# Optimization experiments

Measured on AMD Instinct MI355X. Metric: run time of the kernel, lower is better.

The kernel has to match this reference:

```python
import jax, jax.numpy as jnp
import numpy as np

L, H, D, V, TMAX = 12, 12, 768, 50257, 1024
B, T = 2, 1024
HD = D // H
EPS = 1e-5


def new_gelu(x):
    return 0.5 * x * (1.0 + jnp.tanh(jnp.sqrt(2.0 / jnp.pi) * (x + 0.044715 * x ** 3)))


def layer_norm(x, w, b):
    mu = jnp.mean(x, axis=-1, keepdims=True)
    var = jnp.var(x, axis=-1, keepdims=True)
    return (x - mu) * jax.lax.rsqrt(var + EPS) * w + b


def setup_inputs() -> dict:
    key = jax.random.key(0)
    ks = jax.random.split(key, 12)
    s = 0.02
    return {
        "idx": jax.random.randint(ks[0], (B, T), 0, V),
        "wte": jax.random.normal(ks[1], (V, D), jnp.float32) * s,
        "wpe": jax.random.normal(ks[2], (TMAX, D), jnp.float32) * s,
        "ln1_w": jnp.ones((L, D), jnp.float32),
        "ln1_b": jnp.zeros((L, D), jnp.float32),
        "attn_w": jax.random.normal(ks[3], (L, D, 3 * D), jnp.float32) * s,
        "attn_b": jnp.zeros((L, 3 * D), jnp.float32),
        "proj_w": jax.random.normal(ks[4], (L, D, D), jnp.float32) * (s / jnp.sqrt(2.0 * L)),
        "proj_b": jnp.zeros((L, D), jnp.float32),
        "ln2_w": jnp.ones((L, D), jnp.float32),
        "ln2_b": jnp.zeros((L, D), jnp.float32),
        "fc_w": jax.random.normal(ks[5], (L, D, 4 * D), jnp.float32) * s,
        "fc_b": jnp.zeros((L, 4 * D), jnp.float32),
        "fc2_w": jax.random.normal(ks[6], (L, 4 * D, D), jnp.float32) * (s / jnp.sqrt(2.0 * L)),
        "fc2_b": jnp.zeros((L, D), jnp.float32),
        "lnf_w": jnp.ones((D,), jnp.float32),
        "lnf_b": jnp.zeros((D,), jnp.float32),
        "lm_head_w": jax.random.normal(ks[7], (D, V), jnp.float32) * s,
    }


def _gpt_forward(idx, wte, wpe, ln1_w, ln1_b, attn_w, attn_b, proj_w, proj_b,
                 ln2_w, ln2_b, fc_w, fc_b, fc2_w, fc2_b, lnf_w, lnf_b, lm_head_w):
    b, t = idx.shape
    x = wte[idx] + wpe[:t][None, :, :]  # [B,T,D]
    causal = jnp.tril(jnp.ones((t, t), bool))  # [T,T]
    scale = 1.0 / jnp.sqrt(jnp.asarray(HD, x.dtype))

    layer_params = {
        "ln1_w": ln1_w, "ln1_b": ln1_b, "attn_w": attn_w, "attn_b": attn_b,
        "proj_w": proj_w, "proj_b": proj_b, "ln2_w": ln2_w, "ln2_b": ln2_b,
        "fc_w": fc_w, "fc_b": fc_b, "fc2_w": fc2_w, "fc2_b": fc2_b,
    }

    def block(x, p):
        h = layer_norm(x, p["ln1_w"], p["ln1_b"])
        qkv = h @ p["attn_w"] + p["attn_b"]  # [B,T,3D]
        q, k, v = jnp.split(qkv, 3, axis=-1)
        q = q.reshape(b, t, H, HD)
        k = k.reshape(b, t, H, HD)
        v = v.reshape(b, t, H, HD)
        att = jnp.einsum("bqhd,bkhd->bhqk", q, k) * scale
        att = jnp.where(causal[None, None, :, :], att, -jnp.inf)
        att = jax.nn.softmax(att, axis=-1)
        y = jnp.einsum("bhqk,bkhd->bqhd", att, v).reshape(b, t, D)
        x = x + y @ p["proj_w"] + p["proj_b"]
        h2 = layer_norm(x, p["ln2_w"], p["ln2_b"])
        m = new_gelu(h2 @ p["fc_w"] + p["fc_b"])
        x = x + m @ p["fc2_w"] + p["fc2_b"]
        return x, None

    x, _ = jax.lax.scan(block, x, layer_params)
    x = layer_norm(x, lnf_w, lnf_b)
    logits = x @ lm_head_w  # [B,T,V]
    return logits


def reference(idx, wte, wpe, ln1_w, ln1_b, attn_w, attn_b, proj_w, proj_b,
              ln2_w, ln2_b, fc_w, fc_b, fc2_w, fc2_b, lnf_w, lnf_b, lm_head_w):
    return _gpt_forward(idx, wte, wpe, ln1_w, ln1_b, attn_w, attn_b, proj_w, proj_b,
                        ln2_w, ln2_b, fc_w, fc_b, fc2_w, fc2_b, lnf_w, lnf_b, lm_head_w)
```

## Files before the change

kernel.cpp:

```cpp
#include <hip/hip_runtime.h>
#include <math.h>

#define Bsz  2
#define Tlen 1024
#define Dm   768
#define Hh   12
#define HDm  64
#define Ll   12
#define Vv   50257
#define Mrows (Bsz * Tlen)

typedef __attribute__((ext_vector_type(8))) short short8;
typedef __attribute__((ext_vector_type(4))) float f32x4;

__device__ __forceinline__ float bf2f(unsigned short u) {
  union { unsigned int i; float f; } v; v.i = ((unsigned int)u) << 16; return v.f;
}
__device__ __forceinline__ unsigned short f2bf(float f) {
  union { float f; unsigned int i; } v; v.f = f;
  unsigned int u = v.i;
  return (unsigned short)((u + 0x7FFFu + ((u >> 16) & 1u)) >> 16);
}
__device__ __forceinline__ float gelu_f(float x) {
  const float c = 0.7978845608028654f;
  return 0.5f * x * (1.0f + tanhf(c * (x + 0.044715f * x * x * x)));
}

__device__ __forceinline__ void gl_lds16(const unsigned short* g, unsigned short* l) {
  __builtin_amdgcn_global_load_lds(
      (const __attribute__((address_space(1))) unsigned int*)g,
      (__attribute__((address_space(3))) unsigned int*)l, 16, 0, 0);
}


__global__ void embed_kernel(const int* __restrict__ idx, const float* __restrict__ wte,
                             const float* __restrict__ wpe, float* __restrict__ x) {
  int i = (blockIdx.x * 256 + threadIdx.x) * 4;
  int d = i % Dm;
  int bt = i / Dm;
  int t = bt % Tlen;
  int tok = idx[bt];
  float4 a = *(const float4*)(wte + (size_t)tok * Dm + d);
  float4 p = *(const float4*)(wpe + (size_t)t * Dm + d);
  float4 r; r.x = a.x + p.x; r.y = a.y + p.y; r.z = a.z + p.z; r.w = a.w + p.w;
  *(float4*)(x + i) = r;
}

__global__ __launch_bounds__(256) void ln_wave(const float* __restrict__ x,
                                               const float* __restrict__ w,
                                               const float* __restrict__ b,
                                               unsigned short* __restrict__ out) {
  int tid = threadIdx.x, wv = tid >> 6, l = tid & 63;
  int row = blockIdx.x * 4 + wv;
  const float* xr = x + (size_t)row * Dm;
  float4 v[3];
  float s = 0.f, s2 = 0.f;
#pragma unroll
  for (int i = 0; i < 3; ++i) {
    v[i] = *(const float4*)(xr + l * 4 + i * 256);
    s += v[i].x + v[i].y + v[i].z + v[i].w;
    s2 += v[i].x * v[i].x + v[i].y * v[i].y + v[i].z * v[i].z + v[i].w * v[i].w;
  }
#pragma unroll
  for (int o = 1; o < 64; o <<= 1) {
    s += __shfl_xor(s, o, 64);
    s2 += __shfl_xor(s2, o, 64);
  }
  float mu = s * (1.0f / Dm);
  float var = s2 * (1.0f / Dm) - mu * mu;
  float rstd = rsqrtf(var + 1e-5f);
  unsigned short* yr = out + (size_t)row * Dm;
#pragma unroll
  for (int i = 0; i < 3; ++i) {
    float4 wv4 = *(const float4*)(w + l * 4 + i * 256);
    float4 bv4 = *(const float4*)(b + l * 4 + i * 256);
    ushort4 o4;
    o4.x = f2bf((v[i].x - mu) * rstd * wv4.x + bv4.x);
    o4.y = f2bf((v[i].y - mu) * rstd * wv4.y + bv4.y);
    o4.z = f2bf((v[i].z - mu) * rstd * wv4.z + bv4.z);
    o4.w = f2bf((v[i].w - mu) * rstd * wv4.w + bv4.w);
    *(ushort4*)(yr + l * 4 + i * 256) = o4;
  }
}

__global__ __launch_bounds__(256) void tconv_kernel(const float* __restrict__ W, int ldw,
                                                    int nValid, unsigned short* __restrict__ WT,
                                                    int K) {
  __shared__ float S[32][33];
  int n0 = blockIdx.x * 32, k0 = blockIdx.y * 32;
  int t = threadIdx.x;
  int nc = t & 31, kr0 = t >> 5;
#pragma unroll
  for (int i = 0; i < 4; ++i) {
    int kr = kr0 + i * 8;
    S[kr][nc] = (n0 + nc < nValid) ? W[(size_t)(k0 + kr) * ldw + n0 + nc] : 0.f;
  }
  __syncthreads();
  int r = t >> 3, c4 = (t & 7) * 4;
  ushort4 o;
  o.x = f2bf(S[c4 + 0][r]); o.y = f2bf(S[c4 + 1][r]);
  o.z = f2bf(S[c4 + 2][r]); o.w = f2bf(S[c4 + 3][r]);
  *(ushort4*)(WT + (size_t)(n0 + r) * K + k0 + c4) = o;
}

__global__ __launch_bounds__(256) void tconv4_kernel(
    const float* __restrict__ wA, const float* __restrict__ wP,
    const float* __restrict__ wF, const float* __restrict__ wF2,
    unsigned short* __restrict__ oA, unsigned short* __restrict__ oP,
    unsigned short* __restrict__ oF, unsigned short* __restrict__ oF2) {
  int bid = blockIdx.x;
  const float* W; unsigned short* WT; int ldw, K, ntn, local;
  if (bid < 1728)      { W = wA;  WT = oA;  ldw = 2304; K = 768;  ntn = 72; local = bid; }
  else if (bid < 2304) { W = wP;  WT = oP;  ldw = 768;  K = 768;  ntn = 24; local = bid - 1728; }
  else if (bid < 4608) { W = wF;  WT = oF;  ldw = 3072; K = 768;  ntn = 96; local = bid - 2304; }
  else                 { W = wF2; WT = oF2; ldw = 768;  K = 3072; ntn = 24; local = bid - 4608; }
  int n0 = (local % ntn) * 32, k0 = (local / ntn) * 32;
  __shared__ float S[32][33];
  int t = threadIdx.x;
  int nc = t & 31, kr0 = t >> 5;
#pragma unroll
  for (int i = 0; i < 4; ++i) {
    int kr = kr0 + i * 8;
    S[kr][nc] = W[(size_t)(k0 + kr) * ldw + n0 + nc];
  }
  __syncthreads();
  int r = t >> 3, c4 = (t & 7) * 4;
  ushort4 o;
  o.x = f2bf(S[c4 + 0][r]); o.y = f2bf(S[c4 + 1][r]);
  o.z = f2bf(S[c4 + 2][r]); o.w = f2bf(S[c4 + 3][r]);
  *(ushort4*)(WT + (size_t)(n0 + r) * K + k0 + c4) = o;
}

template<bool XMAP>
__global__ __launch_bounds__(256) void gemm_big(
    const unsigned short* __restrict__ A, const unsigned short* __restrict__ B, int K,
    const float* __restrict__ bias, const float* __restrict__ res,
    float* __restrict__ outF, unsigned short* __restrict__ outB,
    int ldc, int nValid, int act, int nColTiles) {
  int brow, bcol;
  if (XMAP) {
    int b = blockIdx.x, xcd = b & 7, slot = b >> 3;
    bcol = xcd + 8 * (slot >> 4);
    brow = slot & 15;
    if (bcol >= nColTiles) return;
  } else {
    bcol = blockIdx.x; brow = blockIdx.y;
  }
  __shared__ alignas(16) unsigned short As[2][128][32];
  __shared__ alignas(16) unsigned short Bs[2][128][32];
  int tid = threadIdx.x;
  int rowBase = brow * 128, colBase = bcol * 128;
  int w = tid >> 6, l = tid & 63;
  int wr = w >> 1, wc = w & 1;
  int srow = tid >> 2;
  int skk = (((tid & 3) ^ ((tid >> 3) & 3))) * 8;
  const unsigned short* aSrc = A + (size_t)(rowBase + srow) * K + skk;
  const unsigned short* bSrc = B + (size_t)(colBase + srow) * K + skk;

  f32x4 acc[4][4];
#pragma unroll
  for (int m = 0; m < 4; ++m)
#pragma unroll
    for (int n = 0; n < 4; ++n) acc[m][n] = (f32x4){0.f, 0.f, 0.f, 0.f};

  int fr = l & 15, fq = l >> 4;
  int kslot = (fq ^ ((fr >> 1) & 3)) * 8;

  gl_lds16(aSrc, &As[0][w * 16][0]);
  gl_lds16(aSrc + (size_t)64 * K, &As[0][w * 16 + 64][0]);
  gl_lds16(bSrc, &Bs[0][w * 16][0]);
  gl_lds16(bSrc + (size_t)64 * K, &Bs[0][w * 16 + 64][0]);

  int nIt = K >> 5;
  for (int it = 0; it < nIt; ++it) {
    int cur = it & 1;
    int k0 = it * 32;
    if (it + 1 < nIt) {
      int nx = cur ^ 1;
      gl_lds16(aSrc + k0 + 32, &As[nx][w * 16][0]);
      gl_lds16(aSrc + (size_t)64 * K + k0 + 32, &As[nx][w * 16 + 64][0]);
      gl_lds16(bSrc + k0 + 32, &Bs[nx][w * 16][0]);
      gl_lds16(bSrc + (size_t)64 * K + k0 + 32, &Bs[nx][w * 16 + 64][0]);
      asm volatile("s_waitcnt vmcnt(4)" ::: "memory");
    } else {
      asm volatile("s_waitcnt vmcnt(0)" ::: "memory");
    }
    asm volatile("s_barrier" ::: "memory");

    short8 af[4], bfr[4];
#pragma unroll
    for (int m = 0; m < 4; ++m)
      af[m] = *(const short8*)&As[cur][wr * 64 + m * 16 + fr][kslot];
#pragma unroll
    for (int n = 0; n < 4; ++n)
      bfr[n] = *(const short8*)&Bs[cur][wc * 64 + n * 16 + fr][kslot];
#pragma unroll
    for (int m = 0; m < 4; ++m)
#pragma unroll
      for (int n = 0; n < 4; ++n)
        acc[m][n] = __builtin_amdgcn_mfma_f32_16x16x32_bf16(af[m], bfr[n], acc[m][n], 0, 0, 0);
    asm volatile("s_barrier" ::: "memory");
  }

#pragma unroll
  for (int m = 0; m < 4; ++m) {
    int row = rowBase + wr * 64 + m * 16 + fq * 4;
#pragma unroll
    for (int n = 0; n < 4; ++n) {
      int col = colBase + wc * 64 + n * 16 + fr;
      if (col >= nValid) continue;
      float bv = bias ? bias[col] : 0.f;
#pragma unroll
      for (int j = 0; j < 4; ++j) {
        float v = acc[m][n][j] + bv;
        if (act) v = gelu_f(v);
        if (res) v += res[(size_t)(row + j) * ldc + col];
        if (outF) outF[(size_t)(row + j) * ldc + col] = v;
        else      outB[(size_t)(row + j) * ldc + col] = f2bf(v);
      }
    }
  }
}

__global__ __launch_bounds__(256) void gemm_bf16_sm(
    const unsigned short* __restrict__ A, const unsigned short* __restrict__ B, int K,
    const float* __restrict__ bias,
    float* __restrict__ outF, unsigned short* __restrict__ outB,
    int ldc, int act) {
  __shared__ alignas(16) unsigned short As[2][64][32];
  __shared__ alignas(16) unsigned short Bs[2][128][32];
  int tid = threadIdx.x;
  int rowBase = blockIdx.y * 64;
  int colBase = blockIdx.x * 128;
  int w = tid >> 6, l = tid & 63;
  int fr = l & 15, fq = l >> 4;

  int srow = l >> 2;
  int skk = (((l & 3) ^ ((l >> 3) & 3))) * 8;
  const unsigned short* aSrc = A + (size_t)(rowBase + w * 16 + srow) * K + skk;
  const unsigned short* bSrc = B + (size_t)(colBase + w * 16 + srow) * K + skk;
  int kslot = (fq ^ ((fr >> 1) & 3)) * 8;

  f32x4 acc[4][2];
#pragma unroll
  for (int m = 0; m < 4; ++m)
#pragma unroll
    for (int n = 0; n < 2; ++n) acc[m][n] = (f32x4){0.f, 0.f, 0.f, 0.f};

  gl_lds16(aSrc, &As[0][w * 16][0]);
  gl_lds16(bSrc, &Bs[0][w * 16][0]);
  gl_lds16(bSrc + (size_t)64 * K, &Bs[0][w * 16 + 64][0]);

  int nIt = K >> 5;
  for (int it = 0; it < nIt; ++it) {
    int cur = it & 1;
    int k0 = it * 32;
    if (it + 1 < nIt) {
      int nx = cur ^ 1;
      gl_lds16(aSrc + k0 + 32, &As[nx][w * 16][0]);
      gl_lds16(bSrc + k0 + 32, &Bs[nx][w * 16][0]);
      gl_lds16(bSrc + (size_t)64 * K + k0 + 32, &Bs[nx][w * 16 + 64][0]);
      asm volatile("s_waitcnt vmcnt(3)" ::: "memory");
    } else {
      asm volatile("s_waitcnt vmcnt(0)" ::: "memory");
    }
    asm volatile("s_barrier" ::: "memory");

    short8 af[4], bfr[2];
#pragma unroll
    for (int m = 0; m < 4; ++m)
      af[m] = *(const short8*)&As[cur][m * 16 + fr][kslot];
#pragma unroll
    for (int n = 0; n < 2; ++n)
      bfr[n] = *(const short8*)&Bs[cur][w * 32 + n * 16 + fr][kslot];
#pragma unroll
    for (int m = 0; m < 4; ++m)
#pragma unroll
      for (int n = 0; n < 2; ++n)
        acc[m][n] = __builtin_amdgcn_mfma_f32_16x16x32_bf16(af[m], bfr[n], acc[m][n], 0, 0, 0);
    asm volatile("s_barrier" ::: "memory");
  }

#pragma unroll
  for (int m = 0; m < 4; ++m) {
    int row = rowBase + m * 16 + fq * 4;
#pragma unroll
    for (int n = 0; n < 2; ++n) {
      int col = colBase + w * 32 + n * 16 + fr;
      float bv = bias ? bias[col] : 0.f;
#pragma unroll
      for (int j = 0; j < 4; ++j) {
        float v = acc[m][n][j] + bv;
        if (act) v = gelu_f(v);
        if (outF) outF[(size_t)(row + j) * ldc + col] = v;
        else      outB[(size_t)(row + j) * ldc + col] = f2bf(v);
      }
    }
  }
}

__global__ __launch_bounds__(256) void gemm_splitk(
    const unsigned short* __restrict__ A, const unsigned short* __restrict__ B, int K,
    int Klen, const float* __restrict__ bias, float* __restrict__ outF, int ldc) {
  __shared__ alignas(16) unsigned short As[2][64][32];
  __shared__ alignas(16) unsigned short Bs[2][128][32];
  int tid = threadIdx.x;
  int rowBase = blockIdx.y * 64;
  int colBase = blockIdx.x * 128;
  int Koff = blockIdx.z * Klen;
  int w = tid >> 6, l = tid & 63;
  int fr = l & 15, fq = l >> 4;

  int srow = l >> 2;
  int skk = (((l & 3) ^ ((l >> 3) & 3))) * 8;
  const unsigned short* aSrc = A + (size_t)(rowBase + w * 16 + srow) * K + Koff + skk;
  const unsigned short* bSrc = B + (size_t)(colBase + w * 16 + srow) * K + Koff + skk;
  int kslot = (fq ^ ((fr >> 1) & 3)) * 8;

  f32x4 acc[4][2];
#pragma unroll
  for (int m = 0; m < 4; ++m)
#pragma unroll
    for (int n = 0; n < 2; ++n) acc[m][n] = (f32x4){0.f, 0.f, 0.f, 0.f};

  gl_lds16(aSrc, &As[0][w * 16][0]);
  gl_lds16(bSrc, &Bs[0][w * 16][0]);
  gl_lds16(bSrc + (size_t)64 * K, &Bs[0][w * 16 + 64][0]);

  int nIt = Klen >> 5;
  for (int it = 0; it < nIt; ++it) {
    int cur = it & 1;
    int k0 = it * 32;
    if (it + 1 < nIt) {
      int nx = cur ^ 1;
      gl_lds16(aSrc + k0 + 32, &As[nx][w * 16][0]);
      gl_lds16(bSrc + k0 + 32, &Bs[nx][w * 16][0]);
      gl_lds16(bSrc + (size_t)64 * K + k0 + 32, &Bs[nx][w * 16 + 64][0]);
      asm volatile("s_waitcnt vmcnt(3)" ::: "memory");
    } else {
      asm volatile("s_waitcnt vmcnt(0)" ::: "memory");
    }
    asm volatile("s_barrier" ::: "memory");

    short8 af[4], bfr[2];
#pragma unroll
    for (int m = 0; m < 4; ++m)
      af[m] = *(const short8*)&As[cur][m * 16 + fr][kslot];
#pragma unroll
    for (int n = 0; n < 2; ++n)
      bfr[n] = *(const short8*)&Bs[cur][w * 32 + n * 16 + fr][kslot];
#pragma unroll
    for (int m = 0; m < 4; ++m)
#pragma unroll
      for (int n = 0; n < 2; ++n)
        acc[m][n] = __builtin_amdgcn_mfma_f32_16x16x32_bf16(af[m], bfr[n], acc[m][n], 0, 0, 0);
    asm volatile("s_barrier" ::: "memory");
  }

  bool addBias = (blockIdx.z == 0);
#pragma unroll
  for (int m = 0; m < 4; ++m) {
    int row = rowBase + m * 16 + fq * 4;
#pragma unroll
    for (int n = 0; n < 2; ++n) {
      int col = colBase + w * 32 + n * 16 + fr;
      float bv = addBias ? bias[col] : 0.f;
#pragma unroll
      for (int j = 0; j < 4; ++j) {
        unsafeAtomicAdd(&outF[(size_t)(row + j) * ldc + col], acc[m][n][j] + bv);
      }
    }
  }
}

__global__ __launch_bounds__(256) void attn_mfma(const unsigned short* __restrict__ qkv,
                                                 unsigned short* __restrict__ y) {
  int bx = blockIdx.x;
  int qt = 15 - (bx / 24);
  int bh = bx % 24;
  int h  = bh % Hh;
  int b  = bh / Hh;
  int q0 = qt * 64;
  int tid = threadIdx.x;
  int w = tid >> 6, l = tid & 63;
  int g = l >> 4, fr = l & 15;

  __shared__ alignas(16) unsigned short Kl[2][4096];
  __shared__ alignas(16) unsigned short Vt[4096];
  __shared__ alignas(16) unsigned short Pl[4][1024];

  const size_t rs = 3 * Dm;
  const unsigned short* base = qkv + (size_t)(b * Tlen) * rs + h * HDm;

  short8 qf[2];
  {
    const unsigned short* qrow = base + (size_t)(q0 + w * 16 + fr) * rs;
    qf[0] = *(const short8*)(qrow + g * 8);
    qf[1] = *(const short8*)(qrow + g * 8 + 32);
  }

  int vt_t = tid >> 2, vt_dc = tid & 3;
  uint4 v0r, v1r;

  f32x4 oAcc[4];
#pragma unroll
  for (int nd = 0; nd < 4; ++nd) oAcc[nd] = (f32x4){0.f, 0.f, 0.f, 0.f};
  float mRun[4] = {-1e30f, -1e30f, -1e30f, -1e30f};
  float lRun[4] = {0.f, 0.f, 0.f, 0.f};

  unsigned short* Pw = &Pl[w][0];
  int nkt = qt + 1;

  {
#pragma unroll
    for (int i = 0; i < 2; ++i) {
      int c = i * 256 + tid;
      int t = c >> 3, cl = c & 7;
      int dch = cl ^ (t & 7);
      gl_lds16(base + (size_t)t * rs + Dm + dch * 8, &Kl[0][(i * 256 + w * 64) * 8]);
    }
    const unsigned short* p = base + (size_t)vt_t * rs + 2 * Dm + vt_dc * 16;
    v0r = *(const uint4*)p;
    v1r = *(const uint4*)(p + 8);
  }

  for (int kt = 0; kt < nkt; ++kt) {
    int cur = kt & 1;
    int kbase = kt * 64;
    asm volatile("s_waitcnt vmcnt(0)" ::: "memory");
    __builtin_amdgcn_s_barrier();

    {
      union { uint4 u; unsigned short s[8]; } a, bb;
      a.u = v0r; bb.u = v1r;
#pragma unroll
      for (int j = 0; j < 8; ++j) {
        int d = vt_dc * 16 + j;
        Vt[d * 64 + (vt_t ^ ((d & 7) << 3))] = a.s[j];
        int d2 = d + 8;
        Vt[d2 * 64 + (vt_t ^ ((d2 & 7) << 3))] = bb.s[j];
      }
    }
    if (kt + 1 < nkt) {
      int kb = kbase + 64;
#pragma unroll
      for (int i = 0; i < 2; ++i) {
        int c = i * 256 + tid;
        int t = c >> 3, cl = c & 7;
        int dch = cl ^ (t & 7);
        gl_lds16(base + (size_t)(kb + t) * rs + Dm + dch * 8,
                 &Kl[cur ^ 1][(i * 256 + w * 64) * 8]);
      }
      const unsigned short* p = base + (size_t)(kb + vt_t) * rs + 2 * Dm + vt_dc * 16;
      v0r = *(const uint4*)p;
      v1r = *(const uint4*)(p + 8);
    }
    asm volatile("s_waitcnt lgkmcnt(0)" ::: "memory");
    __builtin_amdgcn_s_barrier();

    f32x4 sAcc[4];
#pragma unroll
    for (int nt = 0; nt < 4; ++nt) sAcc[nt] = (f32x4){0.f, 0.f, 0.f, 0.f};
#pragma unroll
    for (int ks = 0; ks < 2; ++ks)
#pragma unroll
      for (int nt = 0; nt < 4; ++nt) {
        int kcol = nt * 16 + fr;
        short8 kf = *(const short8*)&Kl[cur][kcol * 64 + ((g * 8 + ks * 32) ^ ((kcol & 7) << 3))];
        sAcc[nt] = __builtin_amdgcn_mfma_f32_16x16x32_bf16(qf[ks], kf, sAcc[nt], 0, 0, 0);
      }

    float corr[4];
#pragma unroll
    for (int j = 0; j < 4; ++j) {
      int qg = q0 + w * 16 + g * 4 + j;
      float tm = -1e30f;
#pragma unroll
      for (int nt = 0; nt < 4; ++nt) {
        float s = sAcc[nt][j] * 0.125f;
        int tg = kbase + nt * 16 + fr;
        if (tg > qg) s = -1e30f;
        sAcc[nt][j] = s;
        tm = fmaxf(tm, s);
      }
      tm = fmaxf(tm, __shfl_xor(tm, 1, 16));
      tm = fmaxf(tm, __shfl_xor(tm, 2, 16));
      tm = fmaxf(tm, __shfl_xor(tm, 4, 16));
      tm = fmaxf(tm, __shfl_xor(tm, 8, 16));
      float mN = fmaxf(mRun[j], tm);
      corr[j] = __expf(mRun[j] - mN);
      mRun[j] = mN;
      float ps = 0.f;
#pragma unroll
      for (int nt = 0; nt < 4; ++nt) {
        float p = __expf(sAcc[nt][j] - mN);
        sAcc[nt][j] = p;
        ps += p;
      }
      ps += __shfl_xor(ps, 1, 16);
      ps += __shfl_xor(ps, 2, 16);
      ps += __shfl_xor(ps, 4, 16);
      ps += __shfl_xor(ps, 8, 16);
      lRun[j] = lRun[j] * corr[j] + ps;
    }

#pragma unroll
    for (int nt = 0; nt < 4; ++nt)
#pragma unroll
      for (int j = 0; j < 4; ++j) {
        int q = g * 4 + j;
        int t = nt * 16 + fr;
        Pw[q * 64 + (t ^ ((q & 7) << 3))] = f2bf(sAcc[nt][j]);
      }
#pragma unroll
    for (int nd = 0; nd < 4; ++nd)
#pragma unroll
      for (int j = 0; j < 4; ++j) oAcc[nd][j] *= corr[j];

#pragma unroll
    for (int ks = 0; ks < 2; ++ks) {
      short8 pf = *(const short8*)&Pw[fr * 64 + ((g * 8 + ks * 32) ^ ((fr & 7) << 3))];
#pragma unroll
      for (int nd = 0; nd < 4; ++nd) {
        int d = nd * 16 + fr;
        short8 vf = *(const short8*)&Vt[d * 64 + ((g * 8 + ks * 32) ^ ((fr & 7) << 3))];
        oAcc[nd] = __builtin_amdgcn_mfma_f32_16x16x32_bf16(pf, vf, oAcc[nd], 0, 0, 0);
      }
    }
  }

#pragma unroll
  for (int j = 0; j < 4; ++j) {
    float inv = 1.0f / lRun[j];
    int q = q0 + w * 16 + g * 4 + j;
    unsigned short* yr = y + (size_t)(b * Tlen + q) * Dm + h * HDm + fr;
#pragma unroll
    for (int nd = 0; nd < 4; ++nd)
      yr[nd * 16] = f2bf(oAcc[nd][j] * inv);
  }
}

extern "C" void kernel_launch(void* const* d_in, const int* in_sizes, int n_in,
                              void* d_out, int out_size, void* d_ws, size_t ws_size,
                              hipStream_t stream) {
  const int*   idx    = (const int*)d_in[0];
  const float* wte    = (const float*)d_in[1];
  const float* wpe    = (const float*)d_in[2];
  const float* ln1_w  = (const float*)d_in[3];
  const float* ln1_b  = (const float*)d_in[4];
  const float* attn_w = (const float*)d_in[5];
  const float* attn_b = (const float*)d_in[6];
  const float* proj_w = (const float*)d_in[7];
  const float* proj_b = (const float*)d_in[8];
  const float* ln2_w  = (const float*)d_in[9];
  const float* ln2_b  = (const float*)d_in[10];
  const float* fc_w   = (const float*)d_in[11];
  const float* fc_b   = (const float*)d_in[12];
  const float* fc2_w  = (const float*)d_in[13];
  const float* fc2_b  = (const float*)d_in[14];
  const float* lnf_w  = (const float*)d_in[15];
  const float* lnf_b  = (const float*)d_in[16];
  const float* lmw    = (const float*)d_in[17];
  float* out = (float*)d_out;

  float* x = (float*)d_ws;
  unsigned short* qkvb = (unsigned short*)(x + (size_t)Mrows * Dm);
  unsigned short* xb   = qkvb + (size_t)Mrows * 3 * Dm;
  unsigned short* yb   = xb + (size_t)Mrows * Dm;
  unsigned short* mb   = yb + (size_t)Mrows * Dm;
  unsigned short* wbuf = mb + (size_t)Mrows * 4 * Dm;
  unsigned short* wAttn = wbuf;
  unsigned short* wProj = wAttn + (size_t)3 * Dm * Dm;
  unsigned short* wFc   = wProj + (size_t)Dm * Dm;
  unsigned short* wFc2  = wFc + (size_t)4 * Dm * Dm;

  const size_t baseBytes = (size_t)Mrows * Dm * 4 + (size_t)Mrows * 9 * Dm * 2;
  size_t availShorts = (ws_size - baseBytes) / 2;
  long long cc = (long long)(availShorts / Dm) & ~127LL;
  if (cc > 50304) cc = 50304;
  const int chunkCols = (int)cc;

  embed_kernel<<<(Mrows * Dm) / 1024, 256, 0, stream>>>(idx, wte, wpe, x);

  for (int l = 0; l < Ll; ++l) {
    tconv4_kernel<<<6912, 256, 0, stream>>>(
        attn_w + (size_t)l * Dm * 3 * Dm, proj_w + (size_t)l * Dm * Dm,
        fc_w + (size_t)l * Dm * 4 * Dm, fc2_w + (size_t)l * 4 * Dm * Dm,
        wAttn, wProj, wFc, wFc2);

    ln_wave<<<Mrows / 4, 256, 0, stream>>>(x, ln1_w + l * Dm, ln1_b + l * Dm, xb);
    gemm_bf16_sm<<<dim3(18, 32), 256, 0, stream>>>(xb, wAttn, Dm, attn_b + (size_t)l * 3 * Dm,
                                                   nullptr, qkvb, 3 * Dm, 0);
    attn_mfma<<<Bsz * Hh * 16, 256, 0, stream>>>(qkvb, yb);
    gemm_splitk<<<dim3(6, 32, 2), 256, 0, stream>>>(yb, wProj, Dm, Dm / 2,
                                                    proj_b + (size_t)l * Dm, x, Dm);
    ln_wave<<<Mrows / 4, 256, 0, stream>>>(x, ln2_w + l * Dm, ln2_b + l * Dm, xb);
    gemm_bf16_sm<<<dim3(24, 32), 256, 0, stream>>>(xb, wFc, Dm, fc_b + (size_t)l * 4 * Dm,
                                                   nullptr, mb, 4 * Dm, 1);
    gemm_splitk<<<dim3(6, 32, 2), 256, 0, stream>>>(mb, wFc2, 4 * Dm, 2 * Dm,
                                                    fc2_b + (size_t)l * Dm, x, Dm);
  }

  ln_wave<<<Mrows / 4, 256, 0, stream>>>(x, lnf_w, lnf_b, xb);
  for (int base = 0; base < Vv; base += chunkCols) {
    int ncv = Vv - base; if (ncv > chunkCols) ncv = chunkCols;
    int ntiles = (ncv + 127) / 128;
    tconv_kernel<<<dim3((ncv + 31) / 32, 24), 256, 0, stream>>>(lmw + base, Vv, ncv, wbuf, Dm);
    int cpx = (ntiles + 7) / 8;
    gemm_big<true><<<8 * 16 * cpx, 256, 0, stream>>>(
        xb, wbuf, Dm, nullptr, nullptr, out + base, nullptr, Vv, ncv, 0, ntiles);
  }
}
```

Before: 2.166 ms.

## Batch all-layer weight conversion into output buffer and triple-buffer GEMM loads

All twelve layers' weights are now converted to transposed bf16 in one launch instead of one launch per layer. The converted weights are staged in the output buffer, which is later overwritten by the logits. The three GEMM kernels move from double to triple buffering of LDS tiles, prefetching two K-steps ahead with adjusted vmcnt waits to hide more load latency. This costs 50% more LDS per block, which may reduce occupancy, and depends on d_out being at least 12 layers of bf16 weights in size.

After: 2.228 ms. 2.8% more time.

```diff
diff --git a/kernel.cpp b/kernel.cpp
--- a/kernel.cpp
+++ b/kernel.cpp
@@ -9,6 +9,7 @@
 #define Ll   12
 #define Vv   50257
 #define Mrows (Bsz * Tlen)
+#define WPL  7077888
 
 typedef __attribute__((ext_vector_type(8))) short short8;
 typedef __attribute__((ext_vector_type(4))) float f32x4;
@@ -103,17 +104,18 @@
   *(ushort4*)(WT + (size_t)(n0 + r) * K + k0 + c4) = o;
 }
 
-__global__ __launch_bounds__(256) void tconv4_kernel(
-    const float* __restrict__ wA, const float* __restrict__ wP,
-    const float* __restrict__ wF, const float* __restrict__ wF2,
-    unsigned short* __restrict__ oA, unsigned short* __restrict__ oP,
-    unsigned short* __restrict__ oF, unsigned short* __restrict__ oF2) {
+__global__ __launch_bounds__(256) void tconv12_kernel(
+    const float* __restrict__ attn_w, const float* __restrict__ proj_w,
+    const float* __restrict__ fc_w, const float* __restrict__ fc2_w,
+    unsigned short* __restrict__ wAll) {
   int bid = blockIdx.x;
+  int lyr = bid / 6912, rem = bid % 6912;
+  unsigned short* wL = wAll + (size_t)lyr * WPL;
   const float* W; unsigned short* WT; int ldw, K, ntn, local;
-  if (bid < 1728)      { W = wA;  WT = oA;  ldw = 2304; K = 768;  ntn = 72; local = bid; }
-  else if (bid < 2304) { W = wP;  WT = oP;  ldw = 768;  K = 768;  ntn = 24; local = bid - 1728; }
-  else if (bid < 4608) { W = wF;  WT = oF;  ldw = 3072; K = 768;  ntn = 96; local = bid - 2304; }
-  else                 { W = wF2; WT = oF2; ldw = 768;  K = 3072; ntn = 24; local = bid - 4608; }
+  if (rem < 1728)      { W = attn_w + (size_t)lyr * Dm * 3 * Dm; WT = wL;                     ldw = 2304; K = 768;  ntn = 72; local = rem; }
+  else if (rem < 2304) { W = proj_w + (size_t)lyr * Dm * Dm;     WT = wL + 1769472;           ldw = 768;  K = 768;  ntn = 24; local = rem - 1728; }
+  else if (rem < 4608) { W = fc_w + (size_t)lyr * Dm * 4 * Dm;   WT = wL + 1769472 + 589824;  ldw = 3072; K = 768;  ntn = 96; local = rem - 2304; }
+  else                 { W = fc2_w + (size_t)lyr * 4 * Dm * Dm;  WT = wL + 1769472 + 589824 + 2359296; ldw = 768; K = 3072; ntn = 24; local = rem - 4608; }
   int n0 = (local % ntn) * 32, k0 = (local / ntn) * 32;
   __shared__ float S[32][33];
   int t = threadIdx.x;
@@ -146,8 +148,8 @@
   } else {
     bcol = blockIdx.x; brow = blockIdx.y;
   }
-  __shared__ alignas(16) unsigned short As[2][128][32];
-  __shared__ alignas(16) unsigned short Bs[2][128][32];
+  __shared__ alignas(16) unsigned short As[3][128][32];
+  __shared__ alignas(16) unsigned short Bs[3][128][32];
   int tid = threadIdx.x;
   int rowBase = brow * 128, colBase = bcol * 128;
   int w = tid >> 6, l = tid & 63;
@@ -166,21 +168,24 @@
   int fr = l & 15, fq = l >> 4;
   int kslot = (fq ^ ((fr >> 1) & 3)) * 8;
 
-  gl_lds16(aSrc, &As[0][w * 16][0]);
-  gl_lds16(aSrc + (size_t)64 * K, &As[0][w * 16 + 64][0]);
-  gl_lds16(bSrc, &Bs[0][w * 16][0]);
-  gl_lds16(bSrc + (size_t)64 * K, &Bs[0][w * 16 + 64][0]);
+#define STAGE_BIG(t_, buf_)                                              \
+  { int k0_ = (t_) * 32;                                                 \
+    gl_lds16(aSrc + k0_, &As[buf_][w * 16][0]);                          \
+    gl_lds16(aSrc + (size_t)64 * K + k0_, &As[buf_][w * 16 + 64][0]);    \
+    gl_lds16(bSrc + k0_, &Bs[buf_][w * 16][0]);                          \
+    gl_lds16(bSrc + (size_t)64 * K + k0_, &Bs[buf_][w * 16 + 64][0]); }
 
   int nIt = K >> 5;
+  STAGE_BIG(0, 0);
+  STAGE_BIG(1, 1);
+
+  int cur = 0;
   for (int it = 0; it < nIt; ++it) {
-    int cur = it & 1;
-    int k0 = it * 32;
-    if (it + 1 < nIt) {
-      int nx = cur ^ 1;
-      gl_lds16(aSrc + k0 + 32, &As[nx][w * 16][0]);
-      gl_lds16(aSrc + (size_t)64 * K + k0 + 32, &As[nx][w * 16 + 64][0]);
-      gl_lds16(bSrc + k0 + 32, &Bs[nx][w * 16][0]);
-      gl_lds16(bSrc + (size_t)64 * K + k0 + 32, &Bs[nx][w * 16 + 64][0]);
+    if (it + 2 < nIt) {
+      int nxt = cur + 2; if (nxt >= 3) nxt -= 3;
+      STAGE_BIG(it + 2, nxt);
+      asm volatile("s_waitcnt vmcnt(8)" ::: "memory");
+    } else if (it + 1 < nIt) {
       asm volatile("s_waitcnt vmcnt(4)" ::: "memory");
     } else {
       asm volatile("s_waitcnt vmcnt(0)" ::: "memory");
@@ -200,7 +205,9 @@
       for (int n = 0; n < 4; ++n)
         acc[m][n] = __builtin_amdgcn_mfma_f32_16x16x32_bf16(af[m], bfr[n], acc[m][n], 0, 0, 0);
     asm volatile("s_barrier" ::: "memory");
-  }
+    cur = cur + 1; if (cur >= 3) cur = 0;
+  }
+#undef STAGE_BIG
 
 #pragma unroll
   for (int m = 0; m < 4; ++m) {
@@ -227,8 +234,8 @@
     const float* __restrict__ bias,
     float* __restrict__ outF, unsigned short* __restrict__ outB,
     int ldc, int act) {
-  __shared__ alignas(16) unsigned short As[2][64][32];
-  __shared__ alignas(16) unsigned short Bs[2][128][32];
+  __shared__ alignas(16) unsigned short As[3][64][32];
+  __shared__ alignas(16) unsigned short Bs[3][128][32];
   int tid = threadIdx.x;
   int rowBase = blockIdx.y * 64;
   int colBase = blockIdx.x * 128;
@@ -247,19 +254,23 @@
 #pragma unroll
     for (int n = 0; n < 2; ++n) acc[m][n] = (f32x4){0.f, 0.f, 0.f, 0.f};
 
-  gl_lds16(aSrc, &As[0][w * 16][0]);
-  gl_lds16(bSrc, &Bs[0][w * 16][0]);
-  gl_lds16(bSrc + (size_t)64 * K, &Bs[0][w * 16 + 64][0]);
+#define STAGE_SM(t_, buf_)                                               \
+  { int k0_ = (t_) * 32;                                                 \
+    gl_lds16(aSrc + k0_, &As[buf_][w * 16][0]);                          \
+    gl_lds16(bSrc + k0_, &Bs[buf_][w * 16][0]);                          \
+    gl_lds16(bSrc + (size_t)64 * K + k0_, &Bs[buf_][w * 16 + 64][0]); }
 
   int nIt = K >> 5;
+  STAGE_SM(0, 0);
+  STAGE_SM(1, 1);
+
+  int cur = 0;
   for (int it = 0; it < nIt; ++it) {
-    int cur = it & 1;
-    int k0 = it * 32;
-    if (it + 1 < nIt) {
-      int nx = cur ^ 1;
-      gl_lds16(aSrc + k0 + 32, &As[nx][w * 16][0]);
-      gl_lds16(bSrc + k0 + 32, &Bs[nx][w * 16][0]);
-      gl_lds16(bSrc + (size_t)64 * K + k0 + 32, &Bs[nx][w * 16 + 64][0]);
+    if (it + 2 < nIt) {
+      int nxt = cur + 2; if (nxt >= 3) nxt -= 3;
+      STAGE_SM(it + 2, nxt);
+      asm volatile("s_waitcnt vmcnt(6)" ::: "memory");
+    } else if (it + 1 < nIt) {
       asm volatile("s_waitcnt vmcnt(3)" ::: "memory");
     } else {
       asm volatile("s_waitcnt vmcnt(0)" ::: "memory");
@@ -279,7 +290,9 @@
       for (int n = 0; n < 2; ++n)
         acc[m][n] = __builtin_amdgcn_mfma_f32_16x16x32_bf16(af[m], bfr[n], acc[m][n], 0, 0, 0);
     asm volatile("s_barrier" ::: "memory");
-  }
+    cur = cur + 1; if (cur >= 3) cur = 0;
+  }
+#undef STAGE_SM
 
 #pragma unroll
   for (int m = 0; m < 4; ++m) {
@@ -302,8 +315,8 @@
 __global__ __launch_bounds__(256) void gemm_splitk(
     const unsigned short* __restrict__ A, const unsigned short* __restrict__ B, int K,
     int Klen, const float* __restrict__ bias, float* __restrict__ outF, int ldc) {
-  __shared__ alignas(16) unsigned short As[2][64][32];
-  __shared__ alignas(16) unsigned short Bs[2][128][32];
+  __shared__ alignas(16) unsigned short As[3][64][32];
+  __shared__ alignas(16) unsigned short Bs[3][128][32];
   int tid = threadIdx.x;
   int rowBase = blockIdx.y * 64;
   int colBase = blockIdx.x * 128;
@@ -323,19 +336,23 @@
 #pragma unroll
     for (int n = 0; n < 2; ++n) acc[m][n] = (f32x4){0.f, 0.f, 0.f, 0.f};
 
-  gl_lds16(aSrc, &As[0][w * 16][0]);
-  gl_lds16(bSrc, &Bs[0][w * 16][0]);
-  gl_lds16(bSrc + (size_t)64 * K, &Bs[0][w * 16 + 64][0]);
+#define STAGE_SK(t_, buf_)                                               \
+  { int k0_ = (t_) * 32;                                                 \
+    gl_lds16(aSrc + k0_, &As[buf_][w * 16][0]);                          \
+    gl_lds16(bSrc + k0_, &Bs[buf_][w * 16][0]);                          \
+    gl_lds16(bSrc + (size_t)64 * K + k0_, &Bs[buf_][w * 16 + 64][0]); }
 
   int nIt = Klen >> 5;
+  STAGE_SK(0, 0);
+  STAGE_SK(1, 1);
+
+  int cur = 0;
   for (int it = 0; it < nIt; ++it) {
-    int cur = it & 1;
-    int k0 = it * 32;
-    if (it + 1 < nIt) {
-      int nx = cur ^ 1;
-      gl_lds16(aSrc + k0 + 32, &As[nx][w * 16][0]);
-      gl_lds16(bSrc + k0 + 32, &Bs[nx][w * 16][0]);
-      gl_lds16(bSrc + (size_t)64 * K + k0 + 32, &Bs[nx][w * 16 + 64][0]);
+    if (it + 2 < nIt) {
+      int nxt = cur + 2; if (nxt >= 3) nxt -= 3;
+      STAGE_SK(it + 2, nxt);
+      asm volatile("s_waitcnt vmcnt(6)" ::: "memory");
+    } else if (it + 1 < nIt) {
       asm volatile("s_waitcnt vmcnt(3)" ::: "memory");
     } else {
       asm volatile("s_waitcnt vmcnt(0)" ::: "memory");
@@ -355,7 +372,9 @@
       for (int n = 0; n < 2; ++n)
         acc[m][n] = __builtin_amdgcn_mfma_f32_16x16x32_bf16(af[m], bfr[n], acc[m][n], 0, 0, 0);
     asm volatile("s_barrier" ::: "memory");
-  }
+    cur = cur + 1; if (cur >= 3) cur = 0;
+  }
+#undef STAGE_SK
 
   bool addBias = (blockIdx.z == 0);
 #pragma unroll
@@ -569,10 +588,8 @@
   unsigned short* yb   = xb + (size_t)Mrows * Dm;
   unsigned short* mb   = yb + (size_t)Mrows * Dm;
   unsigned short* wbuf = mb + (size_t)Mrows * 4 * Dm;
-  unsigned short* wAttn = wbuf;
-  unsigned short* wProj = wAttn + (size_t)3 * Dm * Dm;
-  unsigned short* wFc   = wProj + (size_t)Dm * Dm;
-  unsigned short* wFc2  = wFc + (size_t)4 * Dm * Dm;
+
+  unsigned short* wAll = (unsigned short*)d_out;
 
   const size_t baseBytes = (size_t)Mrows * Dm * 4 + (size_t)Mrows * 9 * Dm * 2;
   size_t availShorts = (ws_size - baseBytes) / 2;
@@ -581,12 +598,14 @@
   const int chunkCols = (int)cc;
 
   embed_kernel<<<(Mrows * Dm) / 1024, 256, 0, stream>>>(idx, wte, wpe, x);
+  tconv12_kernel<<<6912 * Ll, 256, 0, stream>>>(attn_w, proj_w, fc_w, fc2_w, wAll);
 
   for (int l = 0; l < Ll; ++l) {
-    tconv4_kernel<<<6912, 256, 0, stream>>>(
-        attn_w + (size_t)l * Dm * 3 * Dm, proj_w + (size_t)l * Dm * Dm,
-        fc_w + (size_t)l * Dm * 4 * Dm, fc2_w + (size_t)l * 4 * Dm * Dm,
-        wAttn, wProj, wFc, wFc2);
+    unsigned short* wL    = wAll + (size_t)l * WPL;
+    unsigned short* wAttn = wL;
+    unsigned short* wProj = wL + 1769472;
+    unsigned short* wFc   = wL + 1769472 + 589824;
+    unsigned short* wFc2  = wL + 1769472 + 589824 + 2359296;
 
     ln_wave<<<Mrows / 4, 256, 0, stream>>>(x, ln1_w + l * Dm, ln1_b + l * Dm, xb);
     gemm_bf16_sm<<<dim3(18, 32), 256, 0, stream>>>(xb, wAttn, Dm, attn_b + (size_t)l * 3 * Dm,
```
